# Kernel optimization log

Measured on AMD Instinct MI355X. Metric: run time of the kernel, lower is better.

## Reference

```python
import jax, jax.numpy as jnp
import numpy as np
import math

N_HEADS = 16
D_MODEL = 1024
D_FF = 4096
MAX_REL = 32  # max_relative_position
LN_EPS = 1e-5


def _layernorm(x, g, b):
    m = jnp.mean(x, axis=-1, keepdims=True)
    v = jnp.var(x, axis=-1, keepdims=True)
    return (x - m) * jax.lax.rsqrt(v + LN_EPS) * g + b


def setup_inputs() -> dict:
    key = jax.random.key(0)
    ks = jax.random.split(key, 12)
    D, F = D_MODEL, D_FF
    gain = 1.0 / math.sqrt(2.0)
    xav = lambda k, o, i, g=1.0: jax.random.uniform(k, (o, i), jnp.float32, -1.0, 1.0) * (g * math.sqrt(6.0 / (o + i)))
    return {
        "x": jax.random.normal(ks[0], (2, 2048, D), jnp.float32),
        "wq": xav(ks[1], D, D, gain),
        "wk": xav(ks[2], D, D, gain),
        "wv": xav(ks[3], D, D, gain),
        "wo": xav(ks[4], D, D, gain),
        "wo_b": jnp.zeros((D,), jnp.float32),
        "rel_tab": jax.random.normal(ks[5], (2 * MAX_REL - 1, N_HEADS), jnp.float32) * 0.02,
        "ln1_g": jnp.ones((D,), jnp.float32),
        "ln1_b": jnp.zeros((D,), jnp.float32),
        "ln2_g": jnp.ones((D,), jnp.float32),
        "ln2_b": jnp.zeros((D,), jnp.float32),
        "w1": xav(ks[6], F, D),
        "b1": jnp.zeros((F,), jnp.float32),
        "w2": xav(ks[7], D, F),
        "b2": jnp.zeros((D,), jnp.float32),
    }


def reference(x, wq, wk, wv, wo, wo_b, rel_tab, ln1_g, ln1_b, ln2_g, ln2_b, w1, b1, w2, b2):
    B, S, D = x.shape
    H = N_HEADS
    dk = D // H

    def proj(w):  # torch Linear: x @ w.T, then split heads -> [B,H,S,dk]
        return (x @ w.T).reshape(B, S, H, dk).transpose(0, 2, 1, 3)

    q, k, v = proj(wq), proj(wk), proj(wv)

    # Rotary embeddings (per-head dim), exact interleave-to-block formula from source
    t = jnp.arange(S, dtype=jnp.float32)
    inv_freq = 1.0 / (10000.0 ** (jnp.arange(0, dk, 2, dtype=jnp.float32) / dk))
    freqs = t[:, None] * inv_freq[None, :]  # [S, dk/2]
    cos, sin = jnp.cos(freqs), jnp.sin(freqs)

    def rope(z):
        z1, z2 = z[..., ::2], z[..., 1::2]  # [B,H,S,dk/2]
        return jnp.concatenate([z1 * cos - z2 * sin, z1 * sin + z2 * cos], axis=-1)

    q, k = rope(q), rope(k)

    # Manual attention with learned relative-position bias
    scores = jnp.einsum("bhqd,bhkd->bhqk", q, k) / math.sqrt(dk)
    rel = jnp.arange(S)[:, None] - jnp.arange(S)[None, :]
    rel = jnp.clip(rel, -(MAX_REL - 1), MAX_REL - 1) + (MAX_REL - 1)
    bias = rel_tab[rel]  # [S,S,H]
    scores = scores + jnp.transpose(bias, (2, 0, 1))[None]  # [1,H,S,S]
    attn = jax.nn.softmax(scores, axis=-1)
    o = jnp.einsum("bhqk,bhkd->bhqd", attn, v).transpose(0, 2, 1, 3).reshape(B, S, D)
    o = o @ wo.T + wo_b

    # Post-norm residual block
    h = _layernorm(x + o, ln1_g, ln1_b)
    f = jax.nn.gelu(h @ w1.T + b1, approximate=False) @ w2.T + b2
    return _layernorm(h + f, ln2_g, ln2_b)
```

## Files before the change

kernel.cpp:

```cpp
#include <hip/hip_runtime.h>
#include <stdint.h>

#define MB (1ull << 20)
typedef unsigned short u16;
typedef __attribute__((ext_vector_type(8))) short bf16x8;
typedef __attribute__((ext_vector_type(4))) float f32x4;

__device__ __forceinline__ float b2f(u16 u) {
  union { unsigned int i; float f; } c; c.i = ((unsigned int)u) << 16; return c.f;
}
__device__ __forceinline__ u16 f2b(float f) {
  union { float f; unsigned int i; } c; c.f = f;
  unsigned int r = c.i + 0x7fffu + ((c.i >> 16) & 1u);
  return (u16)(r >> 16);
}
__device__ __forceinline__ void gload16(const void* g, void* l) {
  __builtin_amdgcn_global_load_lds(
      (const __attribute__((address_space(1))) void*)g,
      (__attribute__((address_space(3))) void*)l, 16, 0, 0);
}

__global__ __launch_bounds__(256) void f2b_all(
    const float* __restrict__ x, const float* __restrict__ wq, const float* __restrict__ wk,
    const float* __restrict__ wv, const float* __restrict__ wo, const float* __restrict__ w1,
    const float* __restrict__ w2,
    u16* __restrict__ xb, u16* __restrict__ wqkvb, u16* __restrict__ wob,
    u16* __restrict__ w1b, u16* __restrict__ w2b)
{
  int bid = blockIdx.x;
  const float* src; u16* dst;
  if (bid < 4096)       { src = x;  dst = xb; }
  else if (bid < 5120)  { src = wq; dst = wqkvb;           bid -= 4096; }
  else if (bid < 6144)  { src = wk; dst = wqkvb + 1048576; bid -= 5120; }
  else if (bid < 7168)  { src = wv; dst = wqkvb + 2097152; bid -= 6144; }
  else if (bid < 8192)  { src = wo; dst = wob;             bid -= 7168; }
  else if (bid < 12288) { src = w1; dst = w1b;             bid -= 8192; }
  else                  { src = w2; dst = w2b;             bid -= 12288; }
  int i = (bid * 256 + threadIdx.x) * 4;
  float4 v = *(const float4*)(src + i);
  uint2 ov;
  ov.x = (unsigned)f2b(v.x) | ((unsigned)f2b(v.y) << 16);
  ov.y = (unsigned)f2b(v.z) | ((unsigned)f2b(v.w) << 16);
  *(uint2*)(dst + i) = ov;
}

__global__ __launch_bounds__(256) void rope_tab_kernel(float2* __restrict__ tab) {
  int idx = blockIdx.x * 256 + threadIdx.x;
  int s = idx >> 5, j = idx & 31;
  float inv = exp2f(-(float)j * (13.287712379549449f / 32.0f));
  float sn, cs;
  sincosf((float)s * inv, &sn, &cs);
  tab[idx] = make_float2(cs, sn);
}

template<int EPI, int BM>
__global__ __launch_bounds__(256) void gemm_bt(
    const u16* __restrict__ A, const u16* __restrict__ B,
    u16* __restrict__ C, const float* __restrict__ bias,
    int M, int N, int K)
{
  constexpr int MT = BM / 32;
  __shared__ __align__(16) u16 As[BM * 64];
  __shared__ __align__(16) u16 Bs[128 * 64];
  const int tid = threadIdx.x;
  const int lane = tid & 63, wave = tid >> 6;
  const int lr = lane & 15, lg = lane >> 4;
  const int wm = wave >> 1, wn = wave & 1;

  const int nwg = gridDim.x * gridDim.y;
  const int id = blockIdx.y * gridDim.x + blockIdx.x;
  const int nid = (id & 7) * (nwg >> 3) + (id >> 3);
  const int bx = nid % gridDim.x, by = nid / gridDim.x;

  const int srow = tid >> 3;
  const int scsw = ((tid & 7) * 8) ^ ((srow & 7) << 3);
  const size_t abase = (size_t)(by * BM + srow) * K + scsw;
  const size_t bbase = (size_t)(bx * 128 + srow) * K + scsw;

  int aoff[MT][2], boff[4][2];
  #pragma unroll
  for (int mt = 0; mt < MT; mt++) {
    int row = wm * (BM / 2) + mt * 16 + lr;
    #pragma unroll
    for (int kk = 0; kk < 2; kk++)
      aoff[mt][kk] = row * 64 + ((kk * 32 + lg * 8) ^ ((row & 7) << 3));
  }
  #pragma unroll
  for (int nt = 0; nt < 4; nt++) {
    int row = wn * 64 + nt * 16 + lr;
    #pragma unroll
    for (int kk = 0; kk < 2; kk++)
      boff[nt][kk] = row * 64 + ((kk * 32 + lg * 8) ^ ((row & 7) << 3));
  }

  f32x4 acc[MT][4];
  #pragma unroll
  for (int i = 0; i < MT; i++)
    #pragma unroll
    for (int j = 0; j < 4; j++) acc[i][j] = (f32x4){0.f, 0.f, 0.f, 0.f};

  for (int k0 = 0; k0 < K; k0 += 64) {
    __syncthreads();
    #pragma unroll
    for (int h = 0; h < MT; h++)
      gload16(A + abase + (size_t)(h * 32) * K + k0, &As[h * 2048 + tid * 8]);
    #pragma unroll
    for (int h = 0; h < 4; h++)
      gload16(B + bbase + (size_t)(h * 32) * K + k0, &Bs[h * 2048 + tid * 8]);
    __syncthreads();
    #pragma unroll
    for (int kk = 0; kk < 2; kk++) {
      bf16x8 af[MT], bfr[4];
      #pragma unroll
      for (int mt = 0; mt < MT; mt++) af[mt] = *(const bf16x8*)&As[aoff[mt][kk]];
      #pragma unroll
      for (int nt = 0; nt < 4; nt++) bfr[nt] = *(const bf16x8*)&Bs[boff[nt][kk]];
      #pragma unroll
      for (int mt = 0; mt < MT; mt++)
        #pragma unroll
        for (int nt = 0; nt < 4; nt++)
          acc[mt][nt] = __builtin_amdgcn_mfma_f32_16x16x32_bf16(af[mt], bfr[nt], acc[mt][nt], 0, 0, 0);
    }
  }

  #pragma unroll
  for (int mt = 0; mt < MT; mt++)
    #pragma unroll
    for (int nt = 0; nt < 4; nt++) {
      const int row = by * BM + wm * (BM / 2) + mt * 16 + lg * 4;
      const int col = bx * 128 + wn * 64 + nt * 16 + lr;
      const float bv = (EPI >= 1) ? bias[col] : 0.f;
      #pragma unroll
      for (int r = 0; r < 4; r++) {
        float x = acc[mt][nt][r] + bv;
        if (EPI == 2) x = 0.5f * x * (1.f + erff(x * 0.70710678118654752f));
        C[(size_t)(row + r) * N + col] = f2b(x);
      }
    }
}

__global__ __launch_bounds__(256) void rope_kernel(
    const u16* __restrict__ qp, const u16* __restrict__ kp, int stride,
    const float2* __restrict__ tab, u16* __restrict__ qr, u16* __restrict__ kr)
{
  const int gid = blockIdx.x * 4 + (threadIdx.x >> 6);
  const int lane = threadIdx.x & 63;
  const int s = gid & 2047;
  const int bh = gid >> 11;
  const int h = bh & 15, b = bh >> 4;
  const int j = lane & 31;
  float2 t = tab[s * 32 + j];
  const float cs = t.x, sn = t.y;
  const size_t base = (size_t)(b * 2048 + s) * stride + h * 64;
  unsigned int qv = *(const unsigned int*)(qp + base + 2 * j);
  unsigned int kv = *(const unsigned int*)(kp + base + 2 * j);
  float q1 = b2f((u16)qv), q2 = b2f((u16)(qv >> 16));
  float k1 = b2f((u16)kv), k2 = b2f((u16)(kv >> 16));
  float qo = (lane < 32) ? (q1 * cs - q2 * sn) : (q1 * sn + q2 * cs);
  float ko = (lane < 32) ? (k1 * cs - k2 * sn) : (k1 * sn + k2 * cs);
  qr[(size_t)gid * 64 + lane] = f2b(qo * 0.18033688011112042f);
  kr[(size_t)gid * 64 + lane] = f2b(ko);
}

__global__ __launch_bounds__(256) void vtrans_kernel(
    const u16* __restrict__ vp, int stride, u16* __restrict__ vT)
{
  __shared__ u16 t[64][65];
  const int sc = blockIdx.x & 31;
  const int bh = blockIdx.x >> 5;
  const int h = bh & 15, b = bh >> 4;
  const int tid = threadIdx.x;
  #pragma unroll
  for (int i = 0; i < 16; i++) {
    int idx = i * 256 + tid;
    int sl = idx >> 6, d = idx & 63;
    t[sl][d] = vp[(size_t)(b * 2048 + sc * 64 + sl) * stride + h * 64 + d];
  }
  __syncthreads();
  #pragma unroll
  for (int i = 0; i < 16; i++) {
    int idx = i * 256 + tid;
    int d = idx >> 6, sl = idx & 63;
    vT[((size_t)bh * 64 + d) * 2048 + sc * 64 + sl] = t[sl][d];
  }
}

__global__ __launch_bounds__(256) void attn_kernel(
    const u16* __restrict__ qr, const u16* __restrict__ kr,
    const u16* __restrict__ vT, const float* __restrict__ rel_tab,
    u16* __restrict__ o)
{
  __shared__ __align__(16) u16 Ks[2][64 * 64];
  __shared__ __align__(16) u16 Vs[2][64 * 64];
  __shared__ float bias_s[64];

  const int tid = threadIdx.x;
  const int lane = tid & 63, wave = tid >> 6;
  const int lr = lane & 15, lg = lane >> 4;

  const int id = blockIdx.x;
  const int nid = (id & 7) * 128 + (id >> 3);
  const int bh = nid >> 5, qc = nid & 31;
  const int h = bh & 15, b = bh >> 4;
  const int q0 = qc * 64 + wave * 16;

  if (tid < 63) bias_s[tid] = rel_tab[tid * 16 + h] * 1.4426950408889634f;

  const u16* qb = qr + (size_t)bh * 2048 * 64;
  const u16* kb = kr + (size_t)bh * 2048 * 64;
  const u16* vb = vT + (size_t)bh * 64 * 2048;

  bf16x8 qf[2];
  qf[0] = *(const bf16x8*)(qb + (size_t)(q0 + lr) * 64 + lg * 8);
  qf[1] = *(const bf16x8*)(qb + (size_t)(q0 + lr) * 64 + 32 + lg * 8);

  const int srow = tid >> 3;
  const int scsw = ((tid & 7) * 8) ^ ((srow & 7) << 3);

  int koff[4][2];
  #pragma unroll
  for (int nt = 0; nt < 4; nt++)
    #pragma unroll
    for (int ks = 0; ks < 2; ks++)
      koff[nt][ks] = (nt * 16 + lr) * 64 + ((ks * 32 + lg * 8) ^ ((lr & 7) << 3));

  #pragma unroll
  for (int hh = 0; hh < 2; hh++) {
    gload16(kb + (size_t)(hh * 32 + srow) * 64 + scsw, &Ks[0][hh * 2048 + tid * 8]);
    gload16(vb + (size_t)(hh * 32 + srow) * 2048 + scsw, &Vs[0][hh * 2048 + tid * 8]);
  }

  float mrow = -1e30f;
  f32x4 lvec = (f32x4){0.f, 0.f, 0.f, 0.f};
  f32x4 oacc[4];
  #pragma unroll
  for (int nt = 0; nt < 4; nt++) oacc[nt] = (f32x4){0.f, 0.f, 0.f, 0.f};

  const int idx_lo = 4 * (lr + 16 * ((lg & 1) * 2));
  const int idx_hi = idx_lo + 64;
  const bool hiSel = (lg >= 2);

  int cur = 0;
  for (int kc = 0; kc < 32; kc++) {
    const int k0 = kc * 64;
    __syncthreads();
    if (kc < 31) {
      const int kn = k0 + 64;
      #pragma unroll
      for (int hh = 0; hh < 2; hh++) {
        gload16(kb + (size_t)(kn + hh * 32 + srow) * 64 + scsw, &Ks[cur ^ 1][hh * 2048 + tid * 8]);
        gload16(vb + (size_t)(hh * 32 + srow) * 2048 + kn + scsw, &Vs[cur ^ 1][hh * 2048 + tid * 8]);
      }
    }
    const u16* Kc = Ks[cur];
    const u16* Vc = Vs[cur];

    f32x4 sacc[4];
    #pragma unroll
    for (int nt = 0; nt < 4; nt++) sacc[nt] = (f32x4){0.f, 0.f, 0.f, 0.f};
    __builtin_amdgcn_s_setprio(1);
    #pragma unroll
    for (int ks = 0; ks < 2; ks++)
      #pragma unroll
      for (int nt = 0; nt < 4; nt++) {
        bf16x8 kf = *(const bf16x8*)&Kc[koff[nt][ks]];
        sacc[nt] = __builtin_amdgcn_mfma_f32_16x16x32_bf16(kf, qf[ks], sacc[nt], 0, 0, 0);
      }
    __builtin_amdgcn_s_setprio(0);

    f32x4 pvv[4];
    const int dmin = q0 - k0 - 63, dmax = q0 + 15 - k0;
    if (dmin >= 31 || dmax <= -31) {
      const float c = bias_s[dmin >= 31 ? 62 : 0];
      f32x4 m4;
      #pragma unroll
      for (int i = 0; i < 4; i++)
        m4[i] = fmaxf(fmaxf(sacc[0][i], sacc[1][i]), fmaxf(sacc[2][i], sacc[3][i]));
      float rm = fmaxf(fmaxf(m4[0], m4[1]), fmaxf(m4[2], m4[3])) + c;
      rm = fmaxf(rm, __shfl_xor(rm, 16));
      rm = fmaxf(rm, __shfl_xor(rm, 32));
      if (!__all(rm <= mrow + 11.5f)) {
        float mnew = fmaxf(mrow, rm);
        float sc = exp2f(mrow - mnew);
        lvec *= sc;
        #pragma unroll
        for (int nt = 0; nt < 4; nt++) oacc[nt] *= sc;
        mrow = mnew;
      }
      const float off = c - mrow;
      #pragma unroll
      for (int nt = 0; nt < 4; nt++) pvv[nt] = sacc[nt] + off;
    } else {
      #pragma unroll
      for (int nt = 0; nt < 4; nt++)
        #pragma unroll
        for (int r = 0; r < 4; r++) {
          int d = (q0 + lr) - (k0 + nt * 16 + lg * 4 + r);
          d = d < -31 ? -31 : (d > 31 ? 31 : d);
          pvv[nt][r] = sacc[nt][r] + bias_s[d + 31];
        }
      f32x4 m4;
      #pragma unroll
      for (int i = 0; i < 4; i++)
        m4[i] = fmaxf(fmaxf(pvv[0][i], pvv[1][i]), fmaxf(pvv[2][i], pvv[3][i]));
      float rm = fmaxf(fmaxf(m4[0], m4[1]), fmaxf(m4[2], m4[3]));
      rm = fmaxf(rm, __shfl_xor(rm, 16));
      rm = fmaxf(rm, __shfl_xor(rm, 32));
      if (!__all(rm <= mrow + 11.5f)) {
        float mnew = fmaxf(mrow, rm);
        float sc = exp2f(mrow - mnew);
        lvec *= sc;
        #pragma unroll
        for (int nt = 0; nt < 4; nt++) oacc[nt] *= sc;
        mrow = mnew;
      }
      #pragma unroll
      for (int nt = 0; nt < 4; nt++) pvv[nt] = pvv[nt] - mrow;
    }

    unsigned int pk[4][2];
    #pragma unroll
    for (int nt = 0; nt < 4; nt++) {
      f32x4 p;
      #pragma unroll
      for (int i = 0; i < 4; i++) p[i] = exp2f(pvv[nt][i]);
      lvec += p;
      unsigned int pr0, pr1;
      asm("v_cvt_pk_bf16_f32 %0, %1, %2" : "=v"(pr0) : "v"(p[0]), "v"(p[1]));
      asm("v_cvt_pk_bf16_f32 %0, %1, %2" : "=v"(pr1) : "v"(p[2]), "v"(p[3]));
      pk[nt][0] = pr0;
      pk[nt][1] = pr1;
    }

    __builtin_amdgcn_s_setprio(1);
    #pragma unroll
    for (int ks = 0; ks < 2; ks++) {
      int w0a = __builtin_amdgcn_ds_bpermute(idx_lo, (int)pk[ks * 2][0]);
      int w0b = __builtin_amdgcn_ds_bpermute(idx_lo, (int)pk[ks * 2 + 1][0]);
      int w1a = __builtin_amdgcn_ds_bpermute(idx_lo, (int)pk[ks * 2][1]);
      int w1b = __builtin_amdgcn_ds_bpermute(idx_lo, (int)pk[ks * 2 + 1][1]);
      int w2a = __builtin_amdgcn_ds_bpermute(idx_hi, (int)pk[ks * 2][0]);
      int w2b = __builtin_amdgcn_ds_bpermute(idx_hi, (int)pk[ks * 2 + 1][0]);
      int w3a = __builtin_amdgcn_ds_bpermute(idx_hi, (int)pk[ks * 2][1]);
      int w3b = __builtin_amdgcn_ds_bpermute(idx_hi, (int)pk[ks * 2 + 1][1]);
      int4 bw;
      bw.x = hiSel ? w0b : w0a;
      bw.y = hiSel ? w1b : w1a;
      bw.z = hiSel ? w2b : w2a;
      bw.w = hiSel ? w3b : w3a;
      bf16x8 pf = *(bf16x8*)&bw;
      #pragma unroll
      for (int nt = 0; nt < 4; nt++) {
        bf16x8 vf = *(const bf16x8*)&Vc[koff[nt][ks]];
        oacc[nt] = __builtin_amdgcn_mfma_f32_16x16x32_bf16(vf, pf, oacc[nt], 0, 0, 0);
      }
    }
    __builtin_amdgcn_s_setprio(0);
    cur ^= 1;
  }

  float lpart = (lvec[0] + lvec[1]) + (lvec[2] + lvec[3]);
  lpart += __shfl_xor(lpart, 16);
  lpart += __shfl_xor(lpart, 32);
  const float inv = 1.0f / lpart;
  const size_t obase = (size_t)(b * 2048 + q0 + lr) * 1024 + h * 64;
  #pragma unroll
  for (int nt = 0; nt < 4; nt++) {
    uint2 st;
    st.x = (unsigned)f2b(oacc[nt][0] * inv) | ((unsigned)f2b(oacc[nt][1] * inv) << 16);
    st.y = (unsigned)f2b(oacc[nt][2] * inv) | ((unsigned)f2b(oacc[nt][3] * inv) << 16);
    *(uint2*)(o + obase + nt * 16 + lg * 4) = st;
  }
}

__global__ __launch_bounds__(256) void ln1_kernel(
    const float* __restrict__ x, const u16* __restrict__ ao,
    const float* __restrict__ g, const float* __restrict__ bta,
    u16* __restrict__ hb)
{
  const int row = blockIdx.x, tid = threadIdx.x;
  const int wave = tid >> 6, lane = tid & 63;
  const int c = tid * 4;
  float4 xv = *(const float4*)(x + (size_t)row * 1024 + c);
  uint2 av = *(const uint2*)(ao + (size_t)row * 1024 + c);
  float v0 = xv.x + b2f((u16)av.x);
  float v1 = xv.y + b2f((u16)(av.x >> 16));
  float v2 = xv.z + b2f((u16)av.y);
  float v3 = xv.w + b2f((u16)(av.y >> 16));
  float s = (v0 + v1) + (v2 + v3);
  float s2 = (v0 * v0 + v1 * v1) + (v2 * v2 + v3 * v3);
  #pragma unroll
  for (int off = 32; off >= 1; off >>= 1) { s += __shfl_down(s, off); s2 += __shfl_down(s2, off); }
  __shared__ float rs[4], rs2[4];
  if (lane == 0) { rs[wave] = s; rs2[wave] = s2; }
  __syncthreads();
  s = rs[0] + rs[1] + rs[2] + rs[3];
  s2 = rs2[0] + rs2[1] + rs2[2] + rs2[3];
  float mean = s * (1.f / 1024.f);
  float var = s2 * (1.f / 1024.f) - mean * mean;
  float inv = rsqrtf(var + 1e-5f);
  float4 gv = *(const float4*)(g + c);
  float4 bv = *(const float4*)(bta + c);
  uint2 ov;
  ov.x = (unsigned)f2b((v0 - mean) * inv * gv.x + bv.x) |
         ((unsigned)f2b((v1 - mean) * inv * gv.y + bv.y) << 16);
  ov.y = (unsigned)f2b((v2 - mean) * inv * gv.z + bv.z) |
         ((unsigned)f2b((v3 - mean) * inv * gv.w + bv.w) << 16);
  *(uint2*)(hb + (size_t)row * 1024 + c) = ov;
}

__global__ __launch_bounds__(256) void ln2_kernel(
    const u16* __restrict__ hb, const u16* __restrict__ fb,
    const float* __restrict__ g, const float* __restrict__ bta,
    float* __restrict__ out)
{
  const int row = blockIdx.x, tid = threadIdx.x;
  const int wave = tid >> 6, lane = tid & 63;
  const int c = tid * 4;
  uint2 hv = *(const uint2*)(hb + (size_t)row * 1024 + c);
  uint2 fv = *(const uint2*)(fb + (size_t)row * 1024 + c);
  float v0 = b2f((u16)hv.x) + b2f((u16)fv.x);
  float v1 = b2f((u16)(hv.x >> 16)) + b2f((u16)(fv.x >> 16));
  float v2 = b2f((u16)hv.y) + b2f((u16)fv.y);
  float v3 = b2f((u16)(hv.y >> 16)) + b2f((u16)(fv.y >> 16));
  float s = (v0 + v1) + (v2 + v3);
  float s2 = (v0 * v0 + v1 * v1) + (v2 * v2 + v3 * v3);
  #pragma unroll
  for (int off = 32; off >= 1; off >>= 1) { s += __shfl_down(s, off); s2 += __shfl_down(s2, off); }
  __shared__ float rs[4], rs2[4];
  if (lane == 0) { rs[wave] = s; rs2[wave] = s2; }
  __syncthreads();
  s = rs[0] + rs[1] + rs[2] + rs[3];
  s2 = rs2[0] + rs2[1] + rs2[2] + rs2[3];
  float mean = s * (1.f / 1024.f);
  float var = s2 * (1.f / 1024.f) - mean * mean;
  float inv = rsqrtf(var + 1e-5f);
  float4 gv = *(const float4*)(g + c);
  float4 bv = *(const float4*)(bta + c);
  float4 ov;
  ov.x = (v0 - mean) * inv * gv.x + bv.x;
  ov.y = (v1 - mean) * inv * gv.y + bv.y;
  ov.z = (v2 - mean) * inv * gv.z + bv.z;
  ov.w = (v3 - mean) * inv * gv.w + bv.w;
  *(float4*)(out + (size_t)row * 1024 + c) = ov;
}

extern "C" void kernel_launch(void* const* d_in, const int* in_sizes, int n_in,
                              void* d_out, int out_size, void* d_ws, size_t ws_size,
                              hipStream_t stream)
{
  const float* x    = (const float*)d_in[0];
  const float* wq   = (const float*)d_in[1];
  const float* wk   = (const float*)d_in[2];
  const float* wv   = (const float*)d_in[3];
  const float* wo   = (const float*)d_in[4];
  const float* wo_b = (const float*)d_in[5];
  const float* rel  = (const float*)d_in[6];
  const float* ln1g = (const float*)d_in[7];
  const float* ln1b = (const float*)d_in[8];
  const float* ln2g = (const float*)d_in[9];
  const float* ln2b = (const float*)d_in[10];
  const float* w1   = (const float*)d_in[11];
  const float* b1   = (const float*)d_in[12];
  const float* w2   = (const float*)d_in[13];
  const float* b2   = (const float*)d_in[14];
  float* out = (float*)d_out;
  char* w = (char*)d_ws;

  if (ws_size < (size_t)90 * MB) return;

  u16* xb    = (u16*)(w + 0 * MB);
  u16* wqkvb = (u16*)(w + 8 * MB);
  u16* wob   = (u16*)(w + 14 * MB);
  u16* w1b   = (u16*)(w + 16 * MB);
  u16* w2b   = (u16*)(w + 24 * MB);
  u16* qkv   = (u16*)(w + 32 * MB);
  u16* ob    = (u16*)(w + 32 * MB);
  u16* ao    = (u16*)(w + 40 * MB);
  u16* hb    = (u16*)(w + 48 * MB);
  u16* qrb   = (u16*)(w + 56 * MB);
  u16* krb   = (u16*)(w + 64 * MB);
  u16* vTb   = (u16*)(w + 72 * MB);
  u16* gb    = (u16*)(w + 56 * MB);
  u16* fb    = (u16*)(w + 0 * MB);
  float2* tab = (float2*)(w + 88 * MB);

  const int M = 4096, D = 1024, F = 4096;

  rope_tab_kernel<<<dim3(256), 256, 0, stream>>>(tab);
  f2b_all<<<dim3(16384), 256, 0, stream>>>(x, wq, wk, wv, wo, w1, w2,
                                           xb, wqkvb, wob, w1b, w2b);

  gemm_bt<0, 128><<<dim3(3 * D / 128, M / 128), 256, 0, stream>>>(xb, wqkvb, qkv, nullptr, M, 3 * D, D);

  rope_kernel<<<dim3(16384), 256, 0, stream>>>(qkv, qkv + 1024, 3 * D, tab, qrb, krb);
  vtrans_kernel<<<dim3(1024), 256, 0, stream>>>(qkv + 2048, 3 * D, vTb);

  attn_kernel<<<dim3(1024), 256, 0, stream>>>(qrb, krb, vTb, rel, ob);

  gemm_bt<1, 64><<<dim3(D / 128, M / 64), 256, 0, stream>>>(ob, wob, ao, wo_b, M, D, D);

  ln1_kernel<<<dim3(M), 256, 0, stream>>>(x, ao, ln1g, ln1b, hb);

  gemm_bt<2, 128><<<dim3(F / 128, M / 128), 256, 0, stream>>>(hb, w1b, gb, b1, M, F, D);

  gemm_bt<1, 64><<<dim3(D / 128, M / 64), 256, 0, stream>>>(gb, w2b, fb, b2, M, D, F);

  ln2_kernel<<<dim3(M), 256, 0, stream>>>(hb, fb, ln2g, ln2b, out);
}
```

Measured before the change: 293.2 us.

## Add 256x256-tile 8-wave GEMM with staged LDS prefetch for QKV and FFN1

Introduces a new gemm256 kernel with 256x256 output tiles and 512 threads. It double-buffers LDS, writes it through global_load_lds with an XOR swizzle, and interleaves the next tile's loads with MFMA phases under s_setprio and barriers. An XCD-aware block remap groups workgroups. The kernel replaces the 128-tile GEMM for the QKV projection and the first FFN GEMM, aiming for higher arithmetic intensity and better load/compute overlap. In exchange it uses more registers and LDS, and launches fewer blocks (192 and 256), which may underfill the CUs.

Result: no change. 289.6 us (-1.2%).

```diff
diff --git a/kernel.cpp b/kernel.cpp
--- a/kernel.cpp
+++ b/kernel.cpp
@@ -133,6 +133,131 @@
       #pragma unroll
       for (int r = 0; r < 4; r++) {
         float x = acc[mt][nt][r] + bv;
+        if (EPI == 2) x = 0.5f * x * (1.f + erff(x * 0.70710678118654752f));
+        C[(size_t)(row + r) * N + col] = f2b(x);
+      }
+    }
+}
+
+#define MFMA16(BASE, BF)                                                       \
+  __builtin_amdgcn_s_setprio(1);                                               \
+  _Pragma("unroll")                                                            \
+  for (int mt = 0; mt < 4; mt++)                                               \
+    _Pragma("unroll")                                                          \
+    for (int nt = 0; nt < 4; nt++)                                             \
+      acc[(BASE) + mt][nt] = __builtin_amdgcn_mfma_f32_16x16x32_bf16(          \
+          af[mt], BF[nt], acc[(BASE) + mt][nt], 0, 0, 0);                      \
+  __builtin_amdgcn_s_setprio(0);
+
+#define SA2(bb, eta, kb)                                                             \
+  gload16(Ab + ((size_t)(eta) * 128) * K + (kb), &As[bb][eta][tid * 8]);             \
+  gload16(Ab + ((size_t)(eta) * 128 + 64) * K + (kb), &As[bb][eta][4096 + tid * 8]);
+#define SB2(bb, eta, kb)                                                             \
+  gload16(Bb + ((size_t)(eta) * 128) * K + (kb), &Bs[bb][eta][tid * 8]);             \
+  gload16(Bb + ((size_t)(eta) * 128 + 64) * K + (kb), &Bs[bb][eta][4096 + tid * 8]);
+
+#define SBAR asm volatile("s_barrier" ::: "memory")
+
+template<int EPI>
+__global__ __launch_bounds__(512) void gemm256(
+    const u16* __restrict__ A, const u16* __restrict__ B,
+    u16* __restrict__ C, const float* __restrict__ bias,
+    int M, int N, int K)
+{
+  __shared__ __align__(16) u16 As[2][2][8192];
+  __shared__ __align__(16) u16 Bs[2][2][8192];
+  const int tid = threadIdx.x;
+  const int lane = tid & 63, wave = tid >> 6;
+  const int lr = lane & 15, lg = lane >> 4;
+  const int wm = wave >> 2, wn = wave & 3;
+
+  const int nwg = gridDim.x * gridDim.y;
+  const int id = blockIdx.y * gridDim.x + blockIdx.x;
+  const int nid = (id & 7) * (nwg >> 3) + (id >> 3);
+  const int bx = nid % gridDim.x, by = nid / gridDim.x;
+
+  const int srow = tid >> 3;
+  const int scsw = ((tid & 7) * 8) ^ ((srow & 7) << 3);
+  const u16* Ab = A + (size_t)(by * 256 + srow) * K + scsw;
+  const u16* Bb = B + (size_t)(bx * 256 + srow) * K + scsw;
+
+  int aoff[2][2][4], boff[2][4];
+  #pragma unroll
+  for (int mh = 0; mh < 2; mh++)
+    #pragma unroll
+    for (int kk = 0; kk < 2; kk++)
+      #pragma unroll
+      for (int mt = 0; mt < 4; mt++) {
+        int row = mh * 64 + mt * 16 + lr;
+        aoff[mh][kk][mt] = row * 64 + ((kk * 32 + lg * 8) ^ ((lr & 7) << 3));
+      }
+  #pragma unroll
+  for (int kk = 0; kk < 2; kk++)
+    #pragma unroll
+    for (int nt = 0; nt < 4; nt++) {
+      int row = (wn & 1) * 64 + nt * 16 + lr;
+      boff[kk][nt] = row * 64 + ((kk * 32 + lg * 8) ^ ((lr & 7) << 3));
+    }
+
+  f32x4 acc[8][4];
+  #pragma unroll
+  for (int i = 0; i < 8; i++)
+    #pragma unroll
+    for (int j = 0; j < 4; j++) acc[i][j] = (f32x4){0.f, 0.f, 0.f, 0.f};
+
+  const int NT = K >> 6;
+
+  SB2(0, 0, 0) SB2(0, 1, 0) SA2(0, 0, 0) SA2(0, 1, 0)
+
+  for (int t = 0; t < NT; ++t) {
+    const int c = t & 1, n = c ^ 1;
+    const size_t kb = (size_t)(t + 1) * 64;
+    const bool st = (t + 1 < NT);
+    const u16* Ac = As[c][wm];
+    const u16* Bc = Bs[c][wn >> 1];
+    bf16x8 b0[4], b1[4], af[4];
+
+    asm volatile("s_waitcnt vmcnt(0)" ::: "memory");
+    SBAR;
+    #pragma unroll
+    for (int nt = 0; nt < 4; nt++) b0[nt] = *(const bf16x8*)&Bc[boff[0][nt]];
+    #pragma unroll
+    for (int mt = 0; mt < 4; mt++) af[mt] = *(const bf16x8*)&Ac[aoff[0][0][mt]];
+    if (st) { SB2(n, 0, kb) }
+    MFMA16(0, b0)
+    SBAR;
+    #pragma unroll
+    for (int nt = 0; nt < 4; nt++) b1[nt] = *(const bf16x8*)&Bc[boff[1][nt]];
+    #pragma unroll
+    for (int mt = 0; mt < 4; mt++) af[mt] = *(const bf16x8*)&Ac[aoff[0][1][mt]];
+    if (st) { SA2(n, 0, kb) }
+    SBAR;
+    MFMA16(0, b1)
+    SBAR;
+    #pragma unroll
+    for (int mt = 0; mt < 4; mt++) af[mt] = *(const bf16x8*)&Ac[aoff[1][0][mt]];
+    if (st) { SB2(n, 1, kb) }
+    SBAR;
+    MFMA16(4, b0)
+    SBAR;
+    #pragma unroll
+    for (int mt = 0; mt < 4; mt++) af[mt] = *(const bf16x8*)&Ac[aoff[1][1][mt]];
+    if (st) { SA2(n, 1, kb) }
+    SBAR;
+    MFMA16(4, b1)
+    SBAR;
+  }
+
+  #pragma unroll
+  for (int m8 = 0; m8 < 8; m8++)
+    #pragma unroll
+    for (int nt = 0; nt < 4; nt++) {
+      const int row = by * 256 + wm * 128 + m8 * 16 + lg * 4;
+      const int col = bx * 256 + wn * 64 + nt * 16 + lr;
+      const float bv = (EPI >= 1) ? bias[col] : 0.f;
+      #pragma unroll
+      for (int r = 0; r < 4; r++) {
+        float x = acc[m8][nt][r] + bv;
         if (EPI == 2) x = 0.5f * x * (1.f + erff(x * 0.70710678118654752f));
         C[(size_t)(row + r) * N + col] = f2b(x);
       }
@@ -491,7 +616,7 @@
   f2b_all<<<dim3(16384), 256, 0, stream>>>(x, wq, wk, wv, wo, w1, w2,
                                            xb, wqkvb, wob, w1b, w2b);
 
-  gemm_bt<0, 128><<<dim3(3 * D / 128, M / 128), 256, 0, stream>>>(xb, wqkvb, qkv, nullptr, M, 3 * D, D);
+  gemm256<0><<<dim3(3 * D / 256, M / 256), 512, 0, stream>>>(xb, wqkvb, qkv, nullptr, M, 3 * D, D);
 
   rope_kernel<<<dim3(16384), 256, 0, stream>>>(qkv, qkv + 1024, 3 * D, tab, qrb, krb);
   vtrans_kernel<<<dim3(1024), 256, 0, stream>>>(qkv + 2048, 3 * D, vTb);
@@ -502,7 +627,7 @@
 
   ln1_kernel<<<dim3(M), 256, 0, stream>>>(x, ao, ln1g, ln1b, hb);
 
-  gemm_bt<2, 128><<<dim3(F / 128, M / 128), 256, 0, stream>>>(hb, w1b, gb, b1, M, F, D);
+  gemm256<2><<<dim3(F / 256, M / 256), 512, 0, stream>>>(hb, w1b, gb, b1, M, F, D);
 
   gemm_bt<1, 64><<<dim3(D / 128, M / 64), 256, 0, stream>>>(gb, w2b, fb, b2, M, D, F);
 
```
